# Optimization experiments

Measured on AMD Instinct MI355X. Metric: run time of the kernel, lower is better.

## Reference

```python
import jax, jax.numpy as jnp
import numpy as np

TOP_K = 4
N_GROUP = 4
TOPK_GROUP = 2
ROUTED_SCALE = 2.5


def grouped_matmul(x, w, group_sizes):
    """x: [N, k] rows sorted by expert; w: [E, k, n]; group_sizes: [E] int32."""
    if hasattr(jax.lax, "ragged_dot"):
        return jax.lax.ragged_dot(x, w, group_sizes)
    # Fallback: expert id per row via searchsorted on cumulative counts, masked dense GEMMs.
    eid = jnp.searchsorted(jnp.cumsum(group_sizes), jnp.arange(x.shape[0]), side="right")
    out = jnp.zeros((x.shape[0], w.shape[-1]), x.dtype)
    for e in range(w.shape[0]):
        out = out + jnp.where((eid == e)[:, None], x @ w[e], 0.0)
    return out


def setup_inputs() -> dict:
    key = jax.random.key(0)
    ks = jax.random.split(key, 9)
    b, s, h, i, E = 2, 2048, 1024, 512, 32
    return {
        "hidden_states": jax.random.normal(ks[0], (b, s, h), jnp.float32),
        "gate_weight": jax.random.normal(ks[1], (E, h), jnp.float32) * 0.02,
        "expert_bias": jnp.zeros((E,), jnp.float32),
        "w_gate": jax.random.normal(ks[2], (E, h, i), jnp.float32) * 0.02,
        "w_up": jax.random.normal(ks[3], (E, h, i), jnp.float32) * 0.02,
        "w_down": jax.random.normal(ks[4], (E, i, h), jnp.float32) * 0.02,
        "ws_gate": jax.random.normal(ks[5], (h, i), jnp.float32) * 0.02,
        "ws_up": jax.random.normal(ks[6], (h, i), jnp.float32) * 0.02,
        "ws_down": jax.random.normal(ks[7], (i, h), jnp.float32) * 0.02,
    }


def reference(hidden_states, gate_weight, expert_bias, w_gate, w_up, w_down,
              ws_gate, ws_up, ws_down):
    b, s, h = hidden_states.shape
    E = gate_weight.shape[0]
    x = hidden_states.reshape(-1, h)          # [T, h]
    T = x.shape[0]

    # --- gate (LLaDA2MoeGate) ---
    logits = x.astype(jnp.float32) @ gate_weight.T.astype(jnp.float32)  # [T, E]
    scores = jax.nn.sigmoid(logits)
    s_rt = scores + expert_bias
    # group-limited top-k: score each group by sum of its top-2 experts
    grp = s_rt.reshape(T, N_GROUP, E // N_GROUP)
    grp_score = jax.lax.top_k(grp, 2)[0].sum(-1)                         # [T, G]
    _, gidx = jax.lax.top_k(grp_score, TOPK_GROUP)
    gmask = jnp.zeros((T, N_GROUP), jnp.float32).at[jnp.arange(T)[:, None], gidx].set(1.0)
    smask = jnp.repeat(gmask, E // N_GROUP, axis=1)                      # [T, E]
    masked = jnp.where(smask > 0, s_rt, -jnp.inf)
    _, topk_idx = jax.lax.top_k(masked, TOP_K)                           # [T, K]
    tw = jnp.take_along_axis(scores, topk_idx, axis=1)
    tw = tw / (tw.sum(-1, keepdims=True) + 1e-20) * ROUTED_SCALE         # [T, K]

    # --- moe_infer: sort by expert, grouped GEMMs, unsort + weighted combine ---
    flat = topk_idx.reshape(-1)                                          # [T*K]
    order = jnp.argsort(flat)
    xs = x[order // TOP_K]                                               # [N, h] sorted by expert
    counts = jnp.bincount(flat, length=E).astype(jnp.int32)
    g = grouped_matmul(xs, w_gate, counts)
    u = grouped_matmul(xs, w_up, counts)
    out_s = grouped_matmul(jax.nn.silu(g) * u, w_down, counts)           # [N, h]
    y = jnp.zeros_like(out_s).at[order].set(out_s)                       # unsort
    y = (y.reshape(T, TOP_K, h) * tw[:, :, None]).sum(1)

    # --- shared experts (SwiGLU MLP on identity) ---
    shared = (jax.nn.silu(x @ ws_gate) * (x @ ws_up)) @ ws_down
    y = (y + shared).reshape(b, s, h)
    return y, logits.reshape(b, s, E), topk_idx.reshape(b, s, TOP_K)
```

## Files before the change

kernel.cpp:

```cpp
#include <hip/hip_runtime.h>
#include <stdint.h>

typedef __attribute__((ext_vector_type(8))) short short8;
typedef __attribute__((ext_vector_type(4))) float f32x4;

#define NR_ROUTED 16384
#define NROWS     20480
#define MAXTILES  192

__device__ __forceinline__ float bf2f(unsigned short h) {
  return __uint_as_float(((unsigned)h) << 16);
}
__device__ __forceinline__ unsigned short f2bf(float f) {
  unsigned u = __float_as_uint(f);
  u = (u + 0x7FFFu + ((u >> 16) & 1u)) >> 16;
  return (unsigned short)u;
}

__global__ void tcast_kernel(const float* __restrict__ src0, const float* __restrict__ src1,
                             unsigned short* __restrict__ dst, int Kd, int Nd, int n_off) {
  __shared__ float tl[64][65];
  int tilesK = Kd >> 6;
  int tk = blockIdx.x % tilesK, tn = blockIdx.x / tilesK;
  int e = blockIdx.y;
  const float* src = (e < 32) ? (src0 + (size_t)e * Kd * Nd) : src1;
  int k0 = tk * 64, n0 = tn * 64;
  int tid = threadIdx.x;
#pragma unroll
  for (int p = 0; p < 4; ++p) {
    int f = p * 256 + tid;
    int r = f >> 4, c4 = (f & 15) * 4;
    float4 v = *(const float4*)(src + (size_t)(k0 + r) * Nd + n0 + c4);
    tl[c4 + 0][r] = v.x; tl[c4 + 1][r] = v.y; tl[c4 + 2][r] = v.z; tl[c4 + 3][r] = v.w;
  }
  __syncthreads();
#pragma unroll
  for (int p = 0; p < 4; ++p) {
    int f = p * 256 + tid;
    int n = f >> 4, kc = (f & 15) * 4;
    ushort4 o;
    o.x = f2bf(tl[n][kc + 0]); o.y = f2bf(tl[n][kc + 1]);
    o.z = f2bf(tl[n][kc + 2]); o.w = f2bf(tl[n][kc + 3]);
    *(ushort4*)(dst + ((size_t)e * 1024 + n_off + n0 + n) * Kd + k0 + kc) = o;
  }
}

__global__ void gwt_kernel(const float* __restrict__ gw, float* __restrict__ gwt) {
  int idx = blockIdx.x * 256 + threadIdx.x;
  int e = idx & 31, j4 = idx >> 5;
  float4 v = *(const float4*)(gw + (size_t)e * 1024 + j4 * 4);
  *(float4*)(gwt + ((size_t)j4 * 32 + e) * 4) = v;
}

__global__ __launch_bounds__(256) void routing_kernel(
    const float* __restrict__ x, const float* __restrict__ gwt,
    const float* __restrict__ bias, unsigned short* __restrict__ xb,
    float* __restrict__ logits_out, float* __restrict__ topk_f,
    int* __restrict__ topk_i, float* __restrict__ tw,
    int* __restrict__ counts) {
  int tid = threadIdx.x;
  int tbase = blockIdx.x * 8;
  const float4* xsrc = (const float4*)(x + (size_t)tbase * 1024);
  ushort4* xbd = (ushort4*)(xb + (size_t)tbase * 1024);
#pragma unroll
  for (int p = 0; p < 8; ++p) {
    float4 v = xsrc[p * 256 + tid];
    ushort4 o;
    o.x = f2bf(v.x); o.y = f2bf(v.y); o.z = f2bf(v.z); o.w = f2bf(v.w);
    xbd[p * 256 + tid] = o;
  }
  int lane = tid & 63, w = tid >> 6;
  int tok2 = lane >> 5, e = lane & 31, h = lane & 32;
  int t = tbase + w * 2 + tok2;
  const float* xrow = x + (size_t)t * 1024;
  float acc = 0.f;
#pragma unroll 8
  for (int j = 0; j < 256; ++j) {
    float4 xv = *(const float4*)(xrow + j * 4);
    float4 wv = *(const float4*)(gwt + ((size_t)j * 32 + e) * 4);
    acc += xv.x * wv.x + xv.y * wv.y + xv.z * wv.z + xv.w * wv.w;
  }
  logits_out[(size_t)t * 32 + e] = acc;
  float sg = 1.f / (1.f + expf(-acc));
  float srt = sg + bias[e];
  float m1 = srt, m2 = -1e30f;
#pragma unroll
  for (int off = 1; off < 8; off <<= 1) {
    float o1 = __shfl_xor(m1, off);
    float o2 = __shfl_xor(m2, off);
    if (o1 > m1) { m2 = fmaxf(m1, o2); m1 = o1; }
    else         { m2 = fmaxf(m2, o1); }
  }
  float gsv = m1 + m2;
  float q0 = __shfl(gsv, h + 0), q1 = __shfl(gsv, h + 8);
  float q2 = __shfl(gsv, h + 16), q3 = __shfl(gsv, h + 24);
  int ga = 0; float bv = q0;
  if (q1 > bv) { ga = 1; bv = q1; }
  if (q2 > bv) { ga = 2; bv = q2; }
  if (q3 > bv) { ga = 3; bv = q3; }
  int gb = -1; float bw = -1e30f;
  if (ga != 0) { gb = 0; bw = q0; }
  if (ga != 1 && q1 > bw) { gb = 1; bw = q1; }
  if (ga != 2 && q2 > bw) { gb = 2; bw = q2; }
  if (ga != 3 && q3 > bw) { gb = 3; bw = q3; }
  unsigned allowed = (0xFFu << (ga * 8)) | (0xFFu << (gb * 8));
  unsigned u = __float_as_uint(srt);
  u = (u & 0x80000000u) ? ~u : (u | 0x80000000u);
  unsigned long long key = ((unsigned long long)u << 32) | (unsigned)(31 - e);
  if (!((allowed >> e) & 1u)) key = 0ull;
  unsigned packed = 0;
  float wsum = 0.f;
#pragma unroll
  for (int k = 0; k < 4; ++k) {
    unsigned long long kk = key;
#pragma unroll
    for (int off = 1; off < 32; off <<= 1) {
      unsigned long long o = __shfl_xor(kk, off);
      if (o > kk) kk = o;
    }
    int ek = 31 - (int)(kk & 0xFFFFFFFFull);
    float sge = __shfl(sg, h + ek);
    wsum += sge;
    packed |= (unsigned)ek << (8 * k);
    if (e == ek) key = 0ull;
  }
  float scale = 2.5f / (wsum + 1e-20f);
  int kq = e & 3;
  int myek = (int)((packed >> (8 * kq)) & 0xFFu);
  float mysg = __shfl(sg, h + myek);
  if (e < 4) {
    int t4 = t * 4 + e;
    topk_i[t4] = myek;
    topk_f[t4] = (float)myek;
    tw[t4] = mysg * scale;
    atomicAdd(&counts[myek], 1);
  }
}

__global__ void build_tiles_kernel(const int* __restrict__ counts, int* __restrict__ cursor,
                                   int4* __restrict__ table, int* __restrict__ n_tiles) {
  if (threadIdx.x != 0) return;
  int base = 0, nt = 0;
  for (int e = 0; e < 32; ++e) {
    cursor[e] = base;
    int n = counts[e];
    for (int j = 0; j < n; j += 128) {
      int rem = n - j;
      table[nt] = make_int4(e, base + j, rem < 128 ? rem : 128, 0);
      ++nt;
    }
    base += n;
  }
  for (int j = 0; j < 32; ++j) {
    table[nt] = make_int4(32, NR_ROUTED + j * 128, 128, 0);
    ++nt;
  }
  *n_tiles = nt;
}

__global__ void assign_kernel(const int* __restrict__ topk_i, int* __restrict__ cursor,
                              int* __restrict__ perm, int* __restrict__ pos) {
  int idx = blockIdx.x * 256 + threadIdx.x;
  if (idx < NR_ROUTED) {
    int e = topk_i[idx];
    int p = atomicAdd(&cursor[e], 1);
    perm[p] = idx >> 2;
    pos[idx] = p;
  } else {
    perm[idx] = idx - NR_ROUTED;
  }
}

__global__ __launch_bounds__(256, 2) void gemm_kernel(
    const unsigned short* __restrict__ A, const unsigned short* __restrict__ B,
    unsigned short* __restrict__ C, const int* __restrict__ perm,
    const int4* __restrict__ table, const int* __restrict__ n_tiles,
    int K, int use_perm) {
  __shared__ unsigned short Al[128 * 64];
  __shared__ unsigned short Bl[128 * 64];
  if ((int)blockIdx.x >= *n_tiles) return;
  int4 te = table[blockIdx.x];
  int eidx = te.x, row_start = te.y, nrows = te.z;
  int n0 = blockIdx.y * 128;
  int tid = threadIdx.x, lane = tid & 63, wave = tid >> 6;
  int wr = wave >> 1, wc = wave & 1;

  const unsigned short* aBase[4];
  const unsigned short* bBase[4];
  unsigned short* aL[4];
  unsigned short* bL[4];
#pragma unroll
  for (int i = 0; i < 4; ++i) {
    int s = wave * 64 + i * 256 + lane;
    int row = s >> 3, cseg = s & 7;
    int rowg = row_start + row;
    int tok = use_perm ? perm[rowg] : rowg;
    aBase[i] = A + (size_t)tok * K + cseg * 8;
    bBase[i] = B + (size_t)eidx * 1024 * K + (size_t)(n0 + row) * K + cseg * 8;
    aL[i] = &Al[(wave * 64 + i * 256) * 8];
    bL[i] = &Bl[(wave * 64 + i * 256) * 8];
  }
  f32x4 acc[4][4];
  f32x4 z = {0.f, 0.f, 0.f, 0.f};
#pragma unroll
  for (int a = 0; a < 4; ++a)
#pragma unroll
    for (int b = 0; b < 4; ++b) acc[a][b] = z;

  for (int k0 = 0; k0 < K; k0 += 64) {
#pragma unroll
    for (int i = 0; i < 4; ++i) {
      __builtin_amdgcn_global_load_lds(
          (const __attribute__((address_space(1))) unsigned int*)(aBase[i] + k0),
          (__attribute__((address_space(3))) unsigned int*)aL[i], 16, 0, 0);
      __builtin_amdgcn_global_load_lds(
          (const __attribute__((address_space(1))) unsigned int*)(bBase[i] + k0),
          (__attribute__((address_space(3))) unsigned int*)bL[i], 16, 0, 0);
    }
    asm volatile("s_waitcnt vmcnt(0)" ::: "memory");
    __syncthreads();
#pragma unroll
    for (int ks = 0; ks < 2; ++ks) {
      short8 af[4], bfr[4];
#pragma unroll
      for (int rf = 0; rf < 4; ++rf) {
        int m = wr * 64 + rf * 16 + (lane & 15);
        af[rf] = *(const short8*)&Al[m * 64 + ks * 32 + (lane >> 4) * 8];
      }
#pragma unroll
      for (int cf = 0; cf < 4; ++cf) {
        int n = wc * 64 + cf * 16 + (lane & 15);
        bfr[cf] = *(const short8*)&Bl[n * 64 + ks * 32 + (lane >> 4) * 8];
      }
#pragma unroll
      for (int rf = 0; rf < 4; ++rf)
#pragma unroll
        for (int cf = 0; cf < 4; ++cf)
          acc[rf][cf] = __builtin_amdgcn_mfma_f32_16x16x32_bf16(af[rf], bfr[cf], acc[rf][cf], 0, 0, 0);
    }
    __syncthreads();
  }
  int q = lane >> 4, cl = lane & 15;
#pragma unroll
  for (int rf = 0; rf < 4; ++rf) {
#pragma unroll
    for (int r = 0; r < 4; ++r) {
      int rowl = wr * 64 + rf * 16 + q * 4 + r;
      if (rowl < nrows) {
        size_t rowg = (size_t)(row_start + rowl);
#pragma unroll
        for (int cf = 0; cf < 4; ++cf) {
          int colg = n0 + wc * 64 + cf * 16 + cl;
          C[rowg * 1024 + colg] = f2bf(acc[rf][cf][r]);
        }
      }
    }
  }
}

__global__ void silu_kernel(const unsigned short* __restrict__ gu, unsigned short* __restrict__ act) {
  int idx = blockIdx.x * 256 + threadIdx.x;
  int row = idx >> 7;
  int c = (idx & 127) * 4;
  ushort4 g4 = *(const ushort4*)(gu + (size_t)row * 1024 + c);
  ushort4 u4 = *(const ushort4*)(gu + (size_t)row * 1024 + 512 + c);
  ushort4 o;
  float g, u;
  g = bf2f(g4.x); u = bf2f(u4.x); o.x = f2bf(g / (1.f + expf(-g)) * u);
  g = bf2f(g4.y); u = bf2f(u4.y); o.y = f2bf(g / (1.f + expf(-g)) * u);
  g = bf2f(g4.z); u = bf2f(u4.z); o.z = f2bf(g / (1.f + expf(-g)) * u);
  g = bf2f(g4.w); u = bf2f(u4.w); o.w = f2bf(g / (1.f + expf(-g)) * u);
  *(ushort4*)(act + (size_t)row * 512 + c) = o;
}

__global__ void combine_kernel(const unsigned short* __restrict__ outs,
                               const int* __restrict__ pos, const float* __restrict__ tw,
                               float* __restrict__ y) {
  int t = blockIdx.x, tid = threadIdx.x;
  int c = tid * 4;
  ushort4 sv = *(const ushort4*)(outs + (size_t)(NR_ROUTED + t) * 1024 + c);
  float y0 = bf2f(sv.x), y1 = bf2f(sv.y), y2 = bf2f(sv.z), y3 = bf2f(sv.w);
#pragma unroll
  for (int k = 0; k < 4; ++k) {
    int p = pos[t * 4 + k];
    float w = tw[t * 4 + k];
    ushort4 v = *(const ushort4*)(outs + (size_t)p * 1024 + c);
    y0 += w * bf2f(v.x); y1 += w * bf2f(v.y); y2 += w * bf2f(v.z); y3 += w * bf2f(v.w);
  }
  float4 o = {y0, y1, y2, y3};
  *(float4*)(y + (size_t)t * 1024 + c) = o;
}

extern "C" void kernel_launch(void* const* d_in, const int* in_sizes, int n_in,
                              void* d_out, int out_size, void* d_ws, size_t ws_size,
                              hipStream_t stream) {
  const float* x       = (const float*)d_in[0];
  const float* gw      = (const float*)d_in[1];
  const float* bias    = (const float*)d_in[2];
  const float* w_gate  = (const float*)d_in[3];
  const float* w_up    = (const float*)d_in[4];
  const float* w_down  = (const float*)d_in[5];
  const float* ws_gate = (const float*)d_in[6];
  const float* ws_up   = (const float*)d_in[7];
  const float* ws_down = (const float*)d_in[8];

  char* ws = (char*)d_ws;
  size_t off = 0;
  auto alloc = [&](size_t bytes) {
    void* p = ws + off;
    off = (off + bytes + 255) & ~(size_t)255;
    return p;
  };
  unsigned short* wgu = (unsigned short*)alloc(33ull * 1024 * 1024 * 2);
  unsigned short* wd  = (unsigned short*)alloc(33ull * 1024 * 512 * 2);
  unsigned short* xb  = (unsigned short*)alloc(4096ull * 1024 * 2);
  unsigned short* gu  = (unsigned short*)alloc((size_t)NROWS * 1024 * 2);
  unsigned short* act = (unsigned short*)alloc((size_t)NROWS * 512 * 2);
  float* gwt    = (float*)alloc(32 * 1024 * 4);
  int*   counts = (int*)alloc(32 * 4);
  int*   cursor = (int*)alloc(32 * 4);
  int*   ntiles = (int*)alloc(256);
  int4*  table  = (int4*)alloc(256 * 16);
  int*   perm   = (int*)alloc(NROWS * 4);
  int*   topk_i = (int*)alloc(NR_ROUTED * 4);
  int*   pos    = (int*)alloc(NR_ROUTED * 4);
  float* tw     = (float*)alloc(NR_ROUTED * 4);
  (void)ws_size; (void)in_sizes; (void)n_in; (void)out_size;

  float* out_y      = (float*)d_out;
  float* out_logits = out_y + 4096ull * 1024;
  float* out_topk   = out_logits + 4096ull * 32;

  hipMemsetAsync(counts, 0, 32 * 4, stream);
  gwt_kernel<<<32, 256, 0, stream>>>(gw, gwt);
  tcast_kernel<<<dim3(128, 33), 256, 0, stream>>>(w_gate, ws_gate, wgu, 1024, 512, 0);
  tcast_kernel<<<dim3(128, 33), 256, 0, stream>>>(w_up,   ws_up,   wgu, 1024, 512, 512);
  tcast_kernel<<<dim3(128, 33), 256, 0, stream>>>(w_down, ws_down, wd,  512, 1024, 0);
  routing_kernel<<<512, 256, 0, stream>>>(x, gwt, bias, xb, out_logits, out_topk, topk_i, tw, counts);
  build_tiles_kernel<<<1, 64, 0, stream>>>(counts, cursor, table, ntiles);
  assign_kernel<<<80, 256, 0, stream>>>(topk_i, cursor, perm, pos);
  gemm_kernel<<<dim3(MAXTILES, 8), 256, 0, stream>>>(xb, wgu, gu, perm, table, ntiles, 1024, 1);
  silu_kernel<<<10240, 256, 0, stream>>>(gu, act);
  gemm_kernel<<<dim3(MAXTILES, 8), 256, 0, stream>>>(act, wd, gu, perm, table, ntiles, 512, 0);
  combine_kernel<<<4096, 256, 0, stream>>>(gu, pos, tw, out_y);
}
```

Before: 484.8 us.

## Fuse SiLU into gate/up GEMM epilogue and double-buffer GEMM LDS loads

Gate and up weight rows are interleaved during the bf16 transpose-cast, so each GEMM tile holds adjacent gate/up column pairs. The epilogue then combines them with a lane shuffle and writes the SiLU activation directly, which removes the separate silu kernel and the round trip of the full gate/up intermediate through memory. The GEMM main loop also double-buffers its LDS tiles, issuing the next k-step's global-to-LDS loads before computing on the current buffer. This doubles LDS use per block to 64 KB, which may reduce occupancy, and half the lanes sit idle during the fused epilogue stores.

```diff
diff --git a/kernel.cpp b/kernel.cpp
--- a/kernel.cpp
+++ b/kernel.cpp
@@ -18,7 +18,8 @@
 }
 
 __global__ void tcast_kernel(const float* __restrict__ src0, const float* __restrict__ src1,
-                             unsigned short* __restrict__ dst, int Kd, int Nd, int n_off) {
+                             unsigned short* __restrict__ dst, int Kd, int Nd,
+                             int n_mul, int n_add) {
   __shared__ float tl[64][65];
   int tilesK = Kd >> 6;
   int tk = blockIdx.x % tilesK, tn = blockIdx.x / tilesK;
@@ -41,7 +42,7 @@
     ushort4 o;
     o.x = f2bf(tl[n][kc + 0]); o.y = f2bf(tl[n][kc + 1]);
     o.z = f2bf(tl[n][kc + 2]); o.w = f2bf(tl[n][kc + 3]);
-    *(ushort4*)(dst + ((size_t)e * 1024 + n_off + n0 + n) * Kd + k0 + kc) = o;
+    *(ushort4*)(dst + ((size_t)e * 1024 + (size_t)(n0 + n) * n_mul + n_add) * Kd + k0 + kc) = o;
   }
 }
 
@@ -175,9 +176,9 @@
     const unsigned short* __restrict__ A, const unsigned short* __restrict__ B,
     unsigned short* __restrict__ C, const int* __restrict__ perm,
     const int4* __restrict__ table, const int* __restrict__ n_tiles,
-    int K, int use_perm) {
-  __shared__ unsigned short Al[128 * 64];
-  __shared__ unsigned short Bl[128 * 64];
+    int K, int use_perm, int fuse_silu, int out_stride) {
+  __shared__ unsigned short Al[2 * 128 * 64];
+  __shared__ unsigned short Bl[2 * 128 * 64];
   if ((int)blockIdx.x >= *n_tiles) return;
   int4 te = table[blockIdx.x];
   int eidx = te.x, row_start = te.y, nrows = te.z;
@@ -187,8 +188,7 @@
 
   const unsigned short* aBase[4];
   const unsigned short* bBase[4];
-  unsigned short* aL[4];
-  unsigned short* bL[4];
+  int lOff[4];
 #pragma unroll
   for (int i = 0; i < 4; ++i) {
     int s = wave * 64 + i * 256 + lane;
@@ -197,8 +197,7 @@
     int tok = use_perm ? perm[rowg] : rowg;
     aBase[i] = A + (size_t)tok * K + cseg * 8;
     bBase[i] = B + (size_t)eidx * 1024 * K + (size_t)(n0 + row) * K + cseg * 8;
-    aL[i] = &Al[(wave * 64 + i * 256) * 8];
-    bL[i] = &Bl[(wave * 64 + i * 256) * 8];
+    lOff[i] = (wave * 64 + i * 256) * 8;
   }
   f32x4 acc[4][4];
   f32x4 z = {0.f, 0.f, 0.f, 0.f};
@@ -207,30 +206,48 @@
 #pragma unroll
     for (int b = 0; b < 4; ++b) acc[a][b] = z;
 
-  for (int k0 = 0; k0 < K; k0 += 64) {
-#pragma unroll
-    for (int i = 0; i < 4; ++i) {
-      __builtin_amdgcn_global_load_lds(
-          (const __attribute__((address_space(1))) unsigned int*)(aBase[i] + k0),
-          (__attribute__((address_space(3))) unsigned int*)aL[i], 16, 0, 0);
-      __builtin_amdgcn_global_load_lds(
-          (const __attribute__((address_space(1))) unsigned int*)(bBase[i] + k0),
-          (__attribute__((address_space(3))) unsigned int*)bL[i], 16, 0, 0);
-    }
+  int nsteps = K >> 6;
+#pragma unroll
+  for (int i = 0; i < 4; ++i) {
+    __builtin_amdgcn_global_load_lds(
+        (const __attribute__((address_space(1))) unsigned int*)(aBase[i]),
+        (__attribute__((address_space(3))) unsigned int*)&Al[lOff[i]], 16, 0, 0);
+    __builtin_amdgcn_global_load_lds(
+        (const __attribute__((address_space(1))) unsigned int*)(bBase[i]),
+        (__attribute__((address_space(3))) unsigned int*)&Bl[lOff[i]], 16, 0, 0);
+  }
+  for (int s = 0; s < nsteps; ++s) {
+    int cur = s & 1;
+    const unsigned short* Ac = &Al[cur * (128 * 64)];
+    const unsigned short* Bc = &Bl[cur * (128 * 64)];
     asm volatile("s_waitcnt vmcnt(0)" ::: "memory");
     __syncthreads();
+    if (s + 1 < nsteps) {
+      int ko = (s + 1) << 6;
+      unsigned short* An = &Al[(cur ^ 1) * (128 * 64)];
+      unsigned short* Bn = &Bl[(cur ^ 1) * (128 * 64)];
+#pragma unroll
+      for (int i = 0; i < 4; ++i) {
+        __builtin_amdgcn_global_load_lds(
+            (const __attribute__((address_space(1))) unsigned int*)(aBase[i] + ko),
+            (__attribute__((address_space(3))) unsigned int*)&An[lOff[i]], 16, 0, 0);
+        __builtin_amdgcn_global_load_lds(
+            (const __attribute__((address_space(1))) unsigned int*)(bBase[i] + ko),
+            (__attribute__((address_space(3))) unsigned int*)&Bn[lOff[i]], 16, 0, 0);
+      }
+    }
 #pragma unroll
     for (int ks = 0; ks < 2; ++ks) {
       short8 af[4], bfr[4];
 #pragma unroll
       for (int rf = 0; rf < 4; ++rf) {
         int m = wr * 64 + rf * 16 + (lane & 15);
-        af[rf] = *(const short8*)&Al[m * 64 + ks * 32 + (lane >> 4) * 8];
+        af[rf] = *(const short8*)&Ac[m * 64 + ks * 32 + (lane >> 4) * 8];
       }
 #pragma unroll
       for (int cf = 0; cf < 4; ++cf) {
         int n = wc * 64 + cf * 16 + (lane & 15);
-        bfr[cf] = *(const short8*)&Bl[n * 64 + ks * 32 + (lane >> 4) * 8];
+        bfr[cf] = *(const short8*)&Bc[n * 64 + ks * 32 + (lane >> 4) * 8];
       }
 #pragma unroll
       for (int rf = 0; rf < 4; ++rf)
@@ -238,39 +255,46 @@
         for (int cf = 0; cf < 4; ++cf)
           acc[rf][cf] = __builtin_amdgcn_mfma_f32_16x16x32_bf16(af[rf], bfr[cf], acc[rf][cf], 0, 0, 0);
     }
-    __syncthreads();
   }
   int q = lane >> 4, cl = lane & 15;
-#pragma unroll
-  for (int rf = 0; rf < 4; ++rf) {
-#pragma unroll
-    for (int r = 0; r < 4; ++r) {
-      int rowl = wr * 64 + rf * 16 + q * 4 + r;
-      if (rowl < nrows) {
+  if (fuse_silu) {
+    bool even = (cl & 1) == 0;
+#pragma unroll
+    for (int rf = 0; rf < 4; ++rf) {
+#pragma unroll
+      for (int r = 0; r < 4; ++r) {
+        int rowl = wr * 64 + rf * 16 + q * 4 + r;
         size_t rowg = (size_t)(row_start + rowl);
 #pragma unroll
         for (int cf = 0; cf < 4; ++cf) {
-          int colg = n0 + wc * 64 + cf * 16 + cl;
-          C[rowg * 1024 + colg] = f2bf(acc[rf][cf][r]);
+          float v = acc[rf][cf][r];
+          float other = __shfl_xor(v, 1);
+          if (even && rowl < nrows) {
+            float g = v, u = other;
+            float a = g / (1.f + expf(-g)) * u;
+            int pcol = (n0 >> 1) + wc * 32 + cf * 8 + (cl >> 1);
+            C[rowg * out_stride + pcol] = f2bf(a);
+          }
         }
       }
     }
-  }
-}
-
-__global__ void silu_kernel(const unsigned short* __restrict__ gu, unsigned short* __restrict__ act) {
-  int idx = blockIdx.x * 256 + threadIdx.x;
-  int row = idx >> 7;
-  int c = (idx & 127) * 4;
-  ushort4 g4 = *(const ushort4*)(gu + (size_t)row * 1024 + c);
-  ushort4 u4 = *(const ushort4*)(gu + (size_t)row * 1024 + 512 + c);
-  ushort4 o;
-  float g, u;
-  g = bf2f(g4.x); u = bf2f(u4.x); o.x = f2bf(g / (1.f + expf(-g)) * u);
-  g = bf2f(g4.y); u = bf2f(u4.y); o.y = f2bf(g / (1.f + expf(-g)) * u);
-  g = bf2f(g4.z); u = bf2f(u4.z); o.z = f2bf(g / (1.f + expf(-g)) * u);
-  g = bf2f(g4.w); u = bf2f(u4.w); o.w = f2bf(g / (1.f + expf(-g)) * u);
-  *(ushort4*)(act + (size_t)row * 512 + c) = o;
+  } else {
+#pragma unroll
+    for (int rf = 0; rf < 4; ++rf) {
+#pragma unroll
+      for (int r = 0; r < 4; ++r) {
+        int rowl = wr * 64 + rf * 16 + q * 4 + r;
+        if (rowl < nrows) {
+          size_t rowg = (size_t)(row_start + rowl);
+#pragma unroll
+          for (int cf = 0; cf < 4; ++cf) {
+            int colg = n0 + wc * 64 + cf * 16 + cl;
+            C[rowg * out_stride + colg] = f2bf(acc[rf][cf][r]);
+          }
+        }
+      }
+    }
+  }
 }
 
 __global__ void combine_kernel(const unsigned short* __restrict__ outs,
@@ -333,14 +357,13 @@
 
   hipMemsetAsync(counts, 0, 32 * 4, stream);
   gwt_kernel<<<32, 256, 0, stream>>>(gw, gwt);
-  tcast_kernel<<<dim3(128, 33), 256, 0, stream>>>(w_gate, ws_gate, wgu, 1024, 512, 0);
-  tcast_kernel<<<dim3(128, 33), 256, 0, stream>>>(w_up,   ws_up,   wgu, 1024, 512, 512);
-  tcast_kernel<<<dim3(128, 33), 256, 0, stream>>>(w_down, ws_down, wd,  512, 1024, 0);
+  tcast_kernel<<<dim3(128, 33), 256, 0, stream>>>(w_gate, ws_gate, wgu, 1024, 512, 2, 0);
+  tcast_kernel<<<dim3(128, 33), 256, 0, stream>>>(w_up,   ws_up,   wgu, 1024, 512, 2, 1);
+  tcast_kernel<<<dim3(128, 33), 256, 0, stream>>>(w_down, ws_down, wd,  512, 1024, 1, 0);
   routing_kernel<<<512, 256, 0, stream>>>(x, gwt, bias, xb, out_logits, out_topk, topk_i, tw, counts);
   build_tiles_kernel<<<1, 64, 0, stream>>>(counts, cursor, table, ntiles);
   assign_kernel<<<80, 256, 0, stream>>>(topk_i, cursor, perm, pos);
-  gemm_kernel<<<dim3(MAXTILES, 8), 256, 0, stream>>>(xb, wgu, gu, perm, table, ntiles, 1024, 1);
-  silu_kernel<<<10240, 256, 0, stream>>>(gu, act);
-  gemm_kernel<<<dim3(MAXTILES, 8), 256, 0, stream>>>(act, wd, gu, perm, table, ntiles, 512, 0);
+  gemm_kernel<<<dim3(MAXTILES, 8), 256, 0, stream>>>(xb, wgu, act, perm, table, ntiles, 1024, 1, 1, 512);
+  gemm_kernel<<<dim3(MAXTILES, 8), 256, 0, stream>>>(act, wd, gu, perm, table, ntiles, 512, 0, 0, 1024);
   combine_kernel<<<4096, 256, 0, stream>>>(gu, pos, tw, out_y);
 }
```

Result: slower. 512.4 us (+5.7%).
